# Optimization experiments

Hardware: AMD Instinct MI355X
Metric: run time of the kernel (lower is better)

The kernel has to match this reference:

```python
import jax, jax.numpy as jnp
import numpy as np
import math

L, B, S, D, H, DI, V = 4, 2, 1024, 768, 12, 3072, 512
DK = D // H

def gelu_tanh(x):
    c = math.sqrt(2.0 / math.pi)
    return 0.5 * x * (1.0 + jnp.tanh(c * (x + 0.044715 * x ** 3)))

def layer_norm(x, g, b, eps=1e-5):
    mu = jnp.mean(x, axis=-1, keepdims=True)
    var = jnp.var(x, axis=-1, keepdims=True)
    return (x - mu) * jax.lax.rsqrt(var + eps) * g + b

def setup_inputs() -> dict:
    key = jax.random.key(0)
    ks = jax.random.split(key, 12)
    w = 0.02  # init scale
    return {
        "x": jax.random.randint(ks[0], (B, S), 0, V),
        "embed": jax.random.normal(ks[1], (V, D), jnp.float32) * w,
        "pos_emb": jax.random.normal(ks[2], (S, D), jnp.float32) * w,
        "ln1_g": jnp.ones((L, D), jnp.float32),
        "ln1_b": jnp.zeros((L, D), jnp.float32),
        "wq": jax.random.normal(ks[3], (L, D, D), jnp.float32) * w,
        "bq": jnp.zeros((L, D), jnp.float32),
        "wk": jax.random.normal(ks[4], (L, D, D), jnp.float32) * w,
        "bk": jnp.zeros((L, D), jnp.float32),
        "wv": jax.random.normal(ks[5], (L, D, D), jnp.float32) * w,
        "bv": jnp.zeros((L, D), jnp.float32),
        "wo": jax.random.normal(ks[6], (L, D, D), jnp.float32) * w,
        "bo": jnp.zeros((L, D), jnp.float32),
        "ln2_g": jnp.ones((L, D), jnp.float32),
        "ln2_b": jnp.zeros((L, D), jnp.float32),
        "w_in": jax.random.normal(ks[7], (L, D, DI), jnp.float32) * w,
        "b_in": jnp.zeros((L, DI), jnp.float32),
        "w_out": jax.random.normal(ks[8], (L, DI, D), jnp.float32) * w,
        "b_out": jnp.zeros((L, D), jnp.float32),
        "lnf_g": jnp.ones((D,), jnp.float32),
        "lnf_b": jnp.zeros((D,), jnp.float32),
        "out_w": jax.random.normal(ks[9], (D, V), jnp.float32) * w,
    }

def reference(x, embed, pos_emb, ln1_g, ln1_b, wq, bq, wk, bk, wv, bv, wo, bo,
              ln2_g, ln2_b, w_in, b_in, w_out, b_out, lnf_g, lnf_b, out_w):
    s = x.shape[1]
    h = embed[x] + pos_emb[None, :s]                       # [B,S,D]
    causal = jnp.tril(jnp.ones((s, s), bool))              # True = keep
    scale = 1.0 / math.sqrt(DK)
    for l in range(L):
        a = layer_norm(h, ln1_g[l], ln1_b[l])
        q = (a @ wq[l] + bq[l]).reshape(-1, s, H, DK)
        k = (a @ wk[l] + bk[l]).reshape(-1, s, H, DK)
        v = (a @ wv[l] + bv[l]).reshape(-1, s, H, DK)
        scores = jnp.einsum('bqhd,bkhd->bhqk', q, k) * scale
        scores = jnp.where(causal, scores, -jnp.inf)
        attn = jax.nn.softmax(scores, axis=-1)
        o = jnp.einsum('bhqk,bkhd->bqhd', attn, v).reshape(-1, s, D)
        h = h + o @ wo[l] + bo[l]
        f = layer_norm(h, ln2_g[l], ln2_b[l])
        h = h + gelu_tanh(f @ w_in[l] + b_in[l]) @ w_out[l] + b_out[l]
    h = layer_norm(h, lnf_g, lnf_b)
    return h @ out_w                                       # [B,S,V] logits
```

## Files before the change

kernel.cpp:

```cpp
#include <hip/hip_runtime.h>
#include <hip/hip_bf16.h>


#define TKN    2048
#define DMODEL 768
#define SEQ    1024
#define NH     12
#define DHEAD  64
#define DFF    3072
#define NL     4
#define NVOCAB 512
#define NQKV   2304

typedef unsigned short u16;
typedef __attribute__((ext_vector_type(4))) float f32x4;
typedef __attribute__((ext_vector_type(8))) short short8;
typedef __attribute__((ext_vector_type(4))) unsigned short us4;
typedef __attribute__((ext_vector_type(8))) unsigned short us8;

__device__ __forceinline__ u16 f2bf(float f) {
  unsigned u = __builtin_bit_cast(unsigned, f);
  u += 0x7fffu + ((u >> 16) & 1u);
  return (u16)(u >> 16);
}

__device__ __forceinline__ float bf2f(u16 u) {
  unsigned v = ((unsigned)u) << 16;
  return __builtin_bit_cast(float, v);
}

__device__ __forceinline__ short8 mk8(us4 lo, us4 hi) {
  short8 r;
  r[0] = (short)lo[0]; r[1] = (short)lo[1]; r[2] = (short)lo[2]; r[3] = (short)lo[3];
  r[4] = (short)hi[0]; r[5] = (short)hi[1]; r[6] = (short)hi[2]; r[7] = (short)hi[3];
  return r;
}

__device__ __forceinline__ void gload16(const u16* g, u16* l) {
  __builtin_amdgcn_global_load_lds(
      (const __attribute__((address_space(1))) unsigned int*)g,
      (__attribute__((address_space(3))) unsigned int*)l, 16, 0, 0);
}

__global__ __launch_bounds__(256) void k_ln(const float* __restrict__ h,
                                            const float* __restrict__ gam,
                                            const float* __restrict__ bet,
                                            u16* __restrict__ out) {
  const int w = threadIdx.x >> 6, lane = threadIdx.x & 63;
  const int row = blockIdx.x * 4 + w;
  const float* hr = h + (size_t)row * DMODEL;
  float4 v0 = *(const float4*)(hr + lane * 4);
  float4 v1 = *(const float4*)(hr + 256 + lane * 4);
  float4 v2 = *(const float4*)(hr + 512 + lane * 4);
  float s = v0.x + v0.y + v0.z + v0.w + v1.x + v1.y + v1.z + v1.w
          + v2.x + v2.y + v2.z + v2.w;
#pragma unroll
  for (int off = 32; off > 0; off >>= 1) s += __shfl_xor(s, off);
  float mu = s * (1.0f / DMODEL);
  float d[12] = {v0.x - mu, v0.y - mu, v0.z - mu, v0.w - mu,
                 v1.x - mu, v1.y - mu, v1.z - mu, v1.w - mu,
                 v2.x - mu, v2.y - mu, v2.z - mu, v2.w - mu};
  float q = 0.0f;
#pragma unroll
  for (int i = 0; i < 12; ++i) q += d[i] * d[i];
#pragma unroll
  for (int off = 32; off > 0; off >>= 1) q += __shfl_xor(q, off);
  float rstd = rsqrtf(q * (1.0f / DMODEL) + 1e-5f);
  size_t o = (size_t)row * DMODEL;
#pragma unroll
  for (int j = 0; j < 3; ++j) {
    float4 gv = *(const float4*)(gam + j * 256 + lane * 4);
    float4 bv = *(const float4*)(bet + j * 256 + lane * 4);
    us4 ov;
    ov[0] = f2bf(d[j * 4 + 0] * rstd * gv.x + bv.x);
    ov[1] = f2bf(d[j * 4 + 1] * rstd * gv.y + bv.y);
    ov[2] = f2bf(d[j * 4 + 2] * rstd * gv.z + bv.z);
    ov[3] = f2bf(d[j * 4 + 3] * rstd * gv.w + bv.w);
    *(us4*)(out + o + j * 256 + lane * 4) = ov;
  }
}

__global__ __launch_bounds__(256) void k_pre(const float* __restrict__ wq,
                                             const float* __restrict__ wk,
                                             const float* __restrict__ wv,
                                             const float* __restrict__ wo,
                                             const float* __restrict__ win,
                                             const float* __restrict__ wout,
                                             const float* __restrict__ outw,
                                             const int* __restrict__ x,
                                             const float* __restrict__ emb,
                                             const float* __restrict__ pos,
                                             const float* __restrict__ bq,
                                             const float* __restrict__ bk,
                                             const float* __restrict__ bv,
                                             u16* __restrict__ wqkvT,
                                             u16* __restrict__ woT,
                                             u16* __restrict__ winT,
                                             u16* __restrict__ woutT,
                                             u16* __restrict__ outwT,
                                             float* __restrict__ h,
                                             float* __restrict__ bqkv) {
  const int l = blockIdx.y;
  const int t = blockIdx.x;
  const int tid = threadIdx.x, lane = tid & 63, w = tid >> 6;

  if (t >= 304) {
    if (l != 0) return;
    if (t == 560) {
      for (int i = tid; i < NL * NQKV; i += 256) {
        int ll = i / NQKV, j = i - ll * NQKV;
        float v = j < DMODEL ? bq[ll * DMODEL + j]
                : j < 2 * DMODEL ? bk[ll * DMODEL + j - DMODEL]
                : bv[ll * DMODEL + j - 2 * DMODEL];
        bqkv[i] = v;
      }
      return;
    }
    int e = t - 304;
#pragma unroll
    for (int tt = 0; tt < 2; ++tt) {
      int tok = e * 8 + w * 2 + tt;
      int s = tok & (SEQ - 1);
      int id = x[tok];
      const float* ep = emb + (size_t)id * DMODEL + lane * 4;
      const float* pp = pos + (size_t)s * DMODEL + lane * 4;
      float* hp = h + (size_t)tok * DMODEL + lane * 4;
#pragma unroll
      for (int j = 0; j < 3; ++j) {
        float4 a = *(const float4*)(ep + j * 256);
        float4 b = *(const float4*)(pp + j * 256);
        float4 o = {a.x + b.x, a.y + b.y, a.z + b.z, a.w + b.w};
        *(float4*)(hp + j * 256) = o;
      }
    }
    return;
  }

  const size_t wDD = (size_t)DMODEL * DMODEL, wDF = (size_t)DMODEL * DFF;
  const float* src; u16* dst;
  int ldS, ldD, scol0, n0, k0;
  if (t < 72) {
    int ntile = t >> 1, kc = t & 1;
    int gn0 = ntile * 64, sel = ntile / 12;
    src = (sel == 0 ? wq : sel == 1 ? wk : wv) + l * wDD; ldS = DMODEL;
    dst = wqkvT + l * (size_t)NQKV * DMODEL; ldD = DMODEL;
    scol0 = gn0 - sel * DMODEL; n0 = gn0; k0 = kc * 384;
  } else if (t < 96) {
    int t2 = t - 72, ntile = t2 >> 1, kc = t2 & 1;
    src = wo + l * wDD; ldS = DMODEL;
    dst = woT + l * wDD; ldD = DMODEL;
    scol0 = ntile * 64; n0 = ntile * 64; k0 = kc * 384;
  } else if (t < 192) {
    int t3 = t - 96, ntile = t3 >> 1, kc = t3 & 1;
    src = win + l * wDF; ldS = DFF;
    dst = winT + l * wDF; ldD = DMODEL;
    scol0 = ntile * 64; n0 = ntile * 64; k0 = kc * 384;
  } else if (t < 288) {
    int t4 = t - 192, ntile = t4 >> 3, kc = t4 & 7;
    src = wout + l * wDF; ldS = DMODEL;
    dst = woutT + l * wDF; ldD = DFF;
    scol0 = ntile * 64; n0 = ntile * 64; k0 = kc * 384;
  } else {
    if (l != 0) return;
    int t5 = t - 288, ntile = t5 >> 1, kc = t5 & 1;
    src = outw; ldS = NVOCAB;
    dst = outwT; ldD = DMODEL;
    scol0 = ntile * 64; n0 = ntile * 64; k0 = kc * 384;
  }
  const int R = lane >> 2, c = lane & 3;
#pragma unroll
  for (int ts = 0; ts < 3; ++ts) {
    const int kw = k0 + w * 96 + ts * 32 + c * 8;
    f32x4 v[8];
#pragma unroll
    for (int j = 0; j < 8; ++j)
      v[j] = *(const f32x4*)(src + (size_t)(kw + j) * ldS + scol0 + R * 4);
#pragma unroll
    for (int i = 0; i < 4; ++i) {
      u16 ob[8];
#pragma unroll
      for (int j = 0; j < 8; ++j) ob[j] = f2bf(v[j][i]);
      *(us8*)(dst + (size_t)(n0 + R * 4 + i) * ldD + kw) = *(us8*)ob;
    }
  }
}

template <int EP>
__global__ __launch_bounds__(256) void k_mm(const u16* __restrict__ A,
                                            const u16* __restrict__ BT,
                                            const float* __restrict__ bias,
                                            void* __restrict__ outp,
                                            int N, int K) {
  constexpr int BM = 64, BN = 64, MI = 2, NJ = 2;
  __shared__ __align__(16) u16 As[3][BM * 64];
  __shared__ __align__(16) u16 Bs[3][BN * 64];
  const int nbx = gridDim.x;
  int lin = blockIdx.y * nbx + blockIdx.x;
  const int chunk = (nbx * gridDim.y) >> 3;
  lin = (lin & 7) * chunk + (lin >> 3);
  const int bn = (lin % nbx) * BN, bm = (lin / nbx) * BM;

  const int tid = threadIdx.x, lane = tid & 63, wid = tid >> 6;
  const int g = lane >> 4, fl = lane & 15;
  const int wm = wid >> 1, wn = wid & 1;

  const int srow = wid * 8 + (lane >> 3);
  const int scol = ((lane & 7) ^ (lane >> 3)) << 3;
  const u16* ag = A + (size_t)(bm + srow) * K + scol;
  const u16* bg = BT + (size_t)(bn + srow) * K + scol;

  f32x4 acc[MI][NJ] = {};
  const int sw = (fl & 7) << 4;

  auto stage = [&](int buf, int kk) {
#pragma unroll
    for (int is = 0; is < MI; ++is)
      gload16(ag + kk + (size_t)is * 32 * K, &As[buf][wid * 512 + is * 2048]);
#pragma unroll
    for (int is = 0; is < NJ; ++is)
      gload16(bg + kk + (size_t)is * 32 * K, &Bs[buf][wid * 512 + is * 2048]);
  };

  const int ks = K / gridDim.z;
  const int kb0 = blockIdx.z * ks;
  const int nk = ks >> 6;
  stage(0, kb0);
  stage(1, kb0 + 64);
  asm volatile("s_waitcnt vmcnt(4)" ::: "memory");
  __builtin_amdgcn_s_barrier();

  int cur = 0, sbuf = 2;
  for (int kt = 0; kt < nk; ++kt) {
    if (kt + 2 < nk) {
      stage(sbuf, kb0 + ((kt + 2) << 6));
      sbuf = (sbuf == 2) ? 0 : sbuf + 1;
    }
#pragma unroll
    for (int k0 = 0; k0 < 64; k0 += 32) {
      const int bo = (k0 + 4 * g) * 2;
      short8 af[MI], bf[NJ];
#pragma unroll
      for (int i = 0; i < MI; ++i) {
        const char* base = (const char*)&As[cur][(wm * 32 + i * 16 + fl) * 64];
        af[i] = mk8(*(const us4*)(base + (bo ^ sw)),
                    *(const us4*)(base + ((bo + 32) ^ sw)));
      }
#pragma unroll
      for (int j = 0; j < NJ; ++j) {
        const char* base = (const char*)&Bs[cur][(wn * 32 + j * 16 + fl) * 64];
        bf[j] = mk8(*(const us4*)(base + (bo ^ sw)),
                    *(const us4*)(base + ((bo + 32) ^ sw)));
      }
#pragma unroll
      for (int i = 0; i < MI; ++i)
#pragma unroll
        for (int j = 0; j < NJ; ++j)
          acc[i][j] = __builtin_amdgcn_mfma_f32_16x16x32_bf16(af[i], bf[j], acc[i][j], 0, 0, 0);
    }
    cur = (cur == 2) ? 0 : cur + 1;
    if (kt + 1 < nk) {
      if (kt + 2 < nk)
        asm volatile("s_waitcnt vmcnt(4) lgkmcnt(0)" ::: "memory");
      else
        asm volatile("s_waitcnt vmcnt(0) lgkmcnt(0)" ::: "memory");
      __builtin_amdgcn_s_barrier();
    }
  }

  const int row0 = bm + wm * 32 + 4 * g;
  const int col0 = bn + wn * 32 + fl;
#pragma unroll
  for (int j = 0; j < NJ; ++j) {
    int col = col0 + j * 16;
    float bv = (EP == 3) ? 0.0f : bias[col];
    if (EP == 1 && blockIdx.z != 0) bv = 0.0f;
#pragma unroll
    for (int i = 0; i < MI; ++i) {
#pragma unroll
      for (int r = 0; r < 4; ++r) {
        int row = row0 + i * 16 + r;
        float val = acc[i][j][r] + bv;
        size_t idx = (size_t)row * N + col;
        if (EP == 0) {
          ((u16*)outp)[idx] = f2bf(val);
        } else if (EP == 1) {
          atomicAdd(&((float*)outp)[idx], val);
        } else if (EP == 2) {
          float t = 1.5957691216057308f * (val + 0.044715f * val * val * val);
          ((u16*)outp)[idx] = f2bf(val / (1.0f + __expf(-t)));
        } else if (EP == 3) {
          ((float*)outp)[idx] = val;
        } else {
          int sel = col / DMODEL;
          int cc = col - sel * DMODEL;
          int hh2 = cc >> 6, dk = cc & 63;
          int bb = row >> 10, ss = row & (SEQ - 1);
          if (sel == 0) val *= 0.125f;
          ((u16*)outp)[(size_t)sel * (TKN * DMODEL) +
                       (((size_t)(bb * NH + hh2) * SEQ + ss) << 6) + dk] = f2bf(val);
        }
      }
    }
  }
}

__global__ __launch_bounds__(256) void k_attn(const u16* __restrict__ qh,
                                              u16* __restrict__ pO,
                                              float* __restrict__ pML,
                                              u16* __restrict__ O) {
  __shared__ u16 Vt[DHEAD * 68];
  int bid = blockIdx.x;
  int lin = (bid & 7) * 120 + (bid >> 3);
  const int bh = lin / 40;
  const int idx = lin - bh * 40;
  int qb, sp;
  if (idx < 4)       { qb = idx;                     sp = 0; }
  else if (idx < 12) { qb = 4 + ((idx - 4) >> 1);    sp = (idx - 4) & 1; }
  else if (idx < 24) { int t = idx - 12; qb = 8 + t / 3;  sp = t - (t / 3) * 3; }
  else               { int t = idx - 24; qb = 12 + (t >> 2); sp = t & 3; }
  const int nsp = 1 + (qb >> 2), nt = qb + 1;
  const int t_lo = sp * nt / nsp, t_hi = (sp + 1) * nt / nsp;

  const int b = bh / NH, hh = bh % NH;
  const u16* kh = qh + TKN * DMODEL;
  const u16* vh = qh + 2 * (TKN * DMODEL);
  const size_t headbase = ((size_t)bh * SEQ) << 6;

  const int tid = threadIdx.x, lane = tid & 63, w = tid >> 6;
  const int g = lane >> 4, fl = lane & 15;
  const int qrow = qb * 64 + w * 16 + fl;

  short8 qf[2];
  {
    const u16* qp = qh + headbase + ((size_t)qrow << 6);
#pragma unroll
    for (int hf = 0; hf < 2; ++hf) {
      us4 lo = *(const us4*)(qp + hf * 32 + 4 * g);
      us4 hi = *(const us4*)(qp + hf * 32 + 16 + 4 * g);
      qf[hf] = mk8(lo, hi);
    }
  }

  float m = -1e30f, lsum = 0.0f;
  f32x4 oacc[4] = {};
  const int vr = tid >> 2, vd = (tid & 3) << 4;
  const u16* vbase = vh + headbase + ((size_t)vr << 6) + vd;
  const u16* kbase = kh + headbase;

  {
    const u16* vp = vbase + ((size_t)t_lo << 12);
    us4 vv[4];
#pragma unroll
    for (int qi = 0; qi < 4; ++qi) vv[qi] = *(const us4*)(vp + qi * 4);
#pragma unroll
    for (int qi = 0; qi < 4; ++qi)
#pragma unroll
      for (int i = 0; i < 4; ++i) Vt[(vd + qi * 4 + i) * 68 + vr] = vv[qi][i];
  }
  __syncthreads();

  for (int t64 = t_lo; t64 < t_hi; ++t64) {
    const u16* kb64 = kbase + ((size_t)t64 << 12);
    us4 kv[4][4];
#pragma unroll
    for (int q4 = 0; q4 < 4; ++q4) {
      const u16* kp = kb64 + ((q4 * 16 + fl) << 6);
#pragma unroll
      for (int j = 0; j < 4; ++j) kv[q4][j] = *(const us4*)(kp + j * 16 + 4 * g);
    }
    const bool pf = (t64 + 1 < t_hi);
    us4 vvn[4];
    if (pf) {
      const u16* vp = vbase + ((size_t)(t64 + 1) << 12);
#pragma unroll
      for (int qi = 0; qi < 4; ++qi) vvn[qi] = *(const us4*)(vp + qi * 4);
    }

    f32x4 sfr[4];
    __builtin_amdgcn_s_setprio(1);
#pragma unroll
    for (int sub = 0; sub < 4; ++sub) {
      short8 kf0 = mk8(kv[sub][0], kv[sub][1]);
      short8 kf1 = mk8(kv[sub][2], kv[sub][3]);
      f32x4 s = {};
      s = __builtin_amdgcn_mfma_f32_16x16x32_bf16(kf0, qf[0], s, 0, 0, 0);
      s = __builtin_amdgcn_mfma_f32_16x16x32_bf16(kf1, qf[1], s, 0, 0, 0);
      sfr[sub] = s;
    }
    __builtin_amdgcn_s_setprio(0);

    float sc[16];
    if (t64 == qb) {
#pragma unroll
      for (int sub = 0; sub < 4; ++sub)
#pragma unroll
        for (int r = 0; r < 4; ++r) {
          int key = t64 * 64 + sub * 16 + 4 * g + r;
          sc[sub * 4 + r] = (key <= qrow) ? sfr[sub][r] : -1e30f;
        }
    } else {
#pragma unroll
      for (int sub = 0; sub < 4; ++sub)
#pragma unroll
        for (int r = 0; r < 4; ++r) sc[sub * 4 + r] = sfr[sub][r];
    }
    float pmax = sc[0];
#pragma unroll
    for (int e = 1; e < 16; ++e) pmax = fmaxf(pmax, sc[e]);
    pmax = fmaxf(pmax, __shfl_xor(pmax, 16));
    pmax = fmaxf(pmax, __shfl_xor(pmax, 32));

    float p[16];
    if (__all(pmax <= m + 8.0f)) {
      float ps = 0.0f;
#pragma unroll
      for (int e = 0; e < 16; ++e) { p[e] = __expf(sc[e] - m); ps += p[e]; }
      ps += __shfl_xor(ps, 16);
      ps += __shfl_xor(ps, 32);
      lsum += ps;
    } else {
      float mnew = fmaxf(m, pmax);
      float corr = __expf(m - mnew);
      float ps = 0.0f;
#pragma unroll
      for (int e = 0; e < 16; ++e) { p[e] = __expf(sc[e] - mnew); ps += p[e]; }
      ps += __shfl_xor(ps, 16);
      ps += __shfl_xor(ps, 32);
      lsum = lsum * corr + ps;
      m = mnew;
      float cr[4];
#pragma unroll
      for (int r = 0; r < 4; ++r) cr[r] = __shfl(corr, 4 * g + r);
#pragma unroll
      for (int nb = 0; nb < 4; ++nb)
#pragma unroll
        for (int r = 0; r < 4; ++r) oacc[nb][r] *= cr[r];
    }

    short8 pf0, pf1;
#pragma unroll
    for (int e = 0; e < 8; ++e) { pf0[e] = (short)f2bf(p[e]); pf1[e] = (short)f2bf(p[8 + e]); }

    __builtin_amdgcn_s_setprio(1);
#pragma unroll
    for (int nb = 0; nb < 4; ++nb) {
      const u16* vtp = &Vt[(nb * 16 + fl) * 68 + 4 * g];
      short8 vf0 = mk8(*(const us4*)vtp, *(const us4*)(vtp + 16));
      short8 vf1 = mk8(*(const us4*)(vtp + 32), *(const us4*)(vtp + 48));
      oacc[nb] = __builtin_amdgcn_mfma_f32_16x16x32_bf16(pf0, vf0, oacc[nb], 0, 0, 0);
      oacc[nb] = __builtin_amdgcn_mfma_f32_16x16x32_bf16(pf1, vf1, oacc[nb], 0, 0, 0);
    }
    __builtin_amdgcn_s_setprio(0);

    if (pf) {
      __syncthreads();
#pragma unroll
      for (int qi = 0; qi < 4; ++qi)
#pragma unroll
        for (int i = 0; i < 4; ++i) Vt[(vd + qi * 4 + i) * 68 + vr] = vvn[qi][i];
      __syncthreads();
    }
  }

  if (nsp == 1) {
    float lr[4];
#pragma unroll
    for (int r = 0; r < 4; ++r) lr[r] = __shfl(lsum, 4 * g + r);
    const int orow0 = b * SEQ + qb * 64 + w * 16 + 4 * g;
#pragma unroll
    for (int nb = 0; nb < 4; ++nb) {
      int col = hh * DHEAD + nb * 16 + fl;
#pragma unroll
      for (int r = 0; r < 4; ++r)
        O[(size_t)(orow0 + r) * DMODEL + col] = f2bf(oacc[nb][r] / lr[r]);
    }
  } else {
    const size_t part = ((size_t)bh * 16 + qb) * 4 + sp;
    u16* ob = pO + part * 4096;
    float* ml = pML + part * 128;
#pragma unroll
    for (int nb = 0; nb < 4; ++nb)
#pragma unroll
      for (int r = 0; r < 4; ++r)
        ob[(w * 16 + 4 * g + r) * 64 + nb * 16 + fl] = f2bf(oacc[nb][r]);
    if (g == 0) {
      ml[w * 16 + fl] = m;
      ml[64 + w * 16 + fl] = lsum;
    }
  }
}

__global__ __launch_bounds__(256) void k_ared(const u16* __restrict__ pO,
                                              const float* __restrict__ pML,
                                              u16* __restrict__ O) {
  __shared__ float wgt[4][64];
  __shared__ float iLs[64];
  const int qb = blockIdx.x + 4, bh = blockIdx.y;
  const int nsp = 1 + (qb >> 2);
  const int b = bh / NH, hh = bh % NH;
  const int tid = threadIdx.x;
  const size_t p0 = ((size_t)bh * 16 + qb) * 4;
  if (tid < 64) {
    float M = -1e30f;
    for (int s = 0; s < nsp; ++s) M = fmaxf(M, pML[(p0 + s) * 128 + tid]);
    float L = 0.0f;
    for (int s = 0; s < nsp; ++s) {
      float wv = __expf(pML[(p0 + s) * 128 + tid] - M);
      wgt[s][tid] = wv;
      L += pML[(p0 + s) * 128 + 64 + tid] * wv;
    }
    iLs[tid] = 1.0f / L;
  }
  __syncthreads();
  for (int i = tid; i < 4096; i += 256) {
    int row = i >> 6, d = i & 63;
    float acc = 0.0f;
    for (int s = 0; s < nsp; ++s)
      acc += bf2f(pO[(p0 + s) * 4096 + i]) * wgt[s][row];
    O[(size_t)(b * SEQ + qb * 64 + row) * DMODEL + hh * DHEAD + d] = f2bf(acc * iLs[row]);
  }
}

extern "C" void kernel_launch(void* const* d_in, const int* in_sizes, int n_in,
                              void* d_out, int out_size, void* d_ws, size_t ws_size,
                              hipStream_t stream) {
  const int*   x    = (const int*)d_in[0];
  const float* emb  = (const float*)d_in[1];
  const float* pos  = (const float*)d_in[2];
  const float* ln1g = (const float*)d_in[3];
  const float* ln1b = (const float*)d_in[4];
  const float* wq   = (const float*)d_in[5];
  const float* bq   = (const float*)d_in[6];
  const float* wk   = (const float*)d_in[7];
  const float* bk   = (const float*)d_in[8];
  const float* wv   = (const float*)d_in[9];
  const float* bv   = (const float*)d_in[10];
  const float* wo   = (const float*)d_in[11];
  const float* bo   = (const float*)d_in[12];
  const float* ln2g = (const float*)d_in[13];
  const float* ln2b = (const float*)d_in[14];
  const float* win  = (const float*)d_in[15];
  const float* bin  = (const float*)d_in[16];
  const float* wout = (const float*)d_in[17];
  const float* bout = (const float*)d_in[18];
  const float* lnfg = (const float*)d_in[19];
  const float* lnfb = (const float*)d_in[20];
  const float* outw = (const float*)d_in[21];

  char* w8 = (char*)d_ws;
  float* h    = (float*)(w8);
  u16* abuf   = (u16*)(w8 + 6291456);
  float* pML  = (float*)(w8 + 6291456);
  u16* qkvh   = (u16*)(w8 + 9437184);
  u16* ffbuf  = (u16*)(w8 + 9437184);
  u16* obuf   = (u16*)(w8 + 18874368);
  u16* outwT  = (u16*)(w8 + 22020096);
  float* bqkv = (float*)(w8 + 22806528);
  u16* pO     = (u16*)(w8 + 22843392);
  u16* wqkvT  = (u16*)(w8 + 48009216);
  u16* woT    = (u16*)(w8 + 62164992);
  u16* winT   = (u16*)(w8 + 66883584);
  u16* woutT  = (u16*)(w8 + 85757952);

  const size_t wDD = (size_t)DMODEL * DMODEL, wDF = (size_t)DMODEL * DFF;
  const size_t wQKV = (size_t)NQKV * DMODEL;

  k_pre<<<dim3(561, NL), 256, 0, stream>>>(
      wq, wk, wv, wo, win, wout, outw, x, emb, pos, bq, bk, bv,
      wqkvT, woT, winT, woutT, outwT, h, bqkv);

  for (int l = 0; l < NL; ++l) {
    k_ln<<<TKN / 4, 256, 0, stream>>>(h, ln1g + l * DMODEL, ln1b + l * DMODEL, abuf);
    k_mm<4><<<dim3(NQKV / 64, TKN / 64, 1), 256, 0, stream>>>(
        abuf, wqkvT + l * wQKV, bqkv + l * NQKV, qkvh, NQKV, DMODEL);
    k_attn<<<960, 256, 0, stream>>>(qkvh, pO, pML, obuf);
    k_ared<<<dim3(12, 2 * NH), 256, 0, stream>>>(pO, pML, obuf);
    k_mm<1><<<dim3(DMODEL / 64, TKN / 64, 2), 256, 0, stream>>>(
        obuf, woT + l * wDD, bo + l * DMODEL, h, DMODEL, DMODEL);
    k_ln<<<TKN / 4, 256, 0, stream>>>(h, ln2g + l * DMODEL, ln2b + l * DMODEL, abuf);
    k_mm<2><<<dim3(DFF / 64, TKN / 64, 1), 256, 0, stream>>>(
        abuf, winT + l * wDF, bin + l * DFF, ffbuf, DFF, DMODEL);
    k_mm<1><<<dim3(DMODEL / 64, TKN / 64, 4), 256, 0, stream>>>(
        ffbuf, woutT + l * wDF, bout + l * DMODEL, h, DMODEL, DFF);
  }

  k_ln<<<TKN / 4, 256, 0, stream>>>(h, lnfg, lnfb, abuf);
  k_mm<3><<<dim3(NVOCAB / 64, TKN / 64, 1), 256, 0, stream>>>(
      abuf, outwT, nullptr, d_out, NVOCAB, DMODEL);
}
```

Baseline: 753.1 us.

## Enlarge GEMM M-tile to 128 with double-buffered pipeline and batch pre-kernel loads

Templates the bf16 MFMA GEMM on BM/BN and launches the layer GEMMs with 128x64 tiles, so each wave computes 4x2 MFMA fragments. This raises reuse of each loaded B tile and halves the block count. The shared-memory pipeline drops from three buffers with a two-stage prefetch and hand-tuned vmcnt waits to two buffers with __syncthreads, which frees LDS but may expose more load latency. The weight transpose/convert pre-kernel now issues all three sets of loads before converting, to get more memory-level parallelism.

```diff
diff --git a/kernel.cpp b/kernel.cpp
--- a/kernel.cpp
+++ b/kernel.cpp
@@ -168,32 +168,37 @@
     scol0 = ntile * 64; n0 = ntile * 64; k0 = kc * 384;
   }
   const int R = lane >> 2, c = lane & 3;
+  f32x4 v[3][8];
 #pragma unroll
   for (int ts = 0; ts < 3; ++ts) {
     const int kw = k0 + w * 96 + ts * 32 + c * 8;
-    f32x4 v[8];
 #pragma unroll
     for (int j = 0; j < 8; ++j)
-      v[j] = *(const f32x4*)(src + (size_t)(kw + j) * ldS + scol0 + R * 4);
+      v[ts][j] = *(const f32x4*)(src + (size_t)(kw + j) * ldS + scol0 + R * 4);
+  }
+#pragma unroll
+  for (int ts = 0; ts < 3; ++ts) {
+    const int kw = k0 + w * 96 + ts * 32 + c * 8;
 #pragma unroll
     for (int i = 0; i < 4; ++i) {
       u16 ob[8];
 #pragma unroll
-      for (int j = 0; j < 8; ++j) ob[j] = f2bf(v[j][i]);
+      for (int j = 0; j < 8; ++j) ob[j] = f2bf(v[ts][j][i]);
       *(us8*)(dst + (size_t)(n0 + R * 4 + i) * ldD + kw) = *(us8*)ob;
     }
   }
 }
 
-template <int EP>
+template <int EP, int BM, int BN>
 __global__ __launch_bounds__(256) void k_mm(const u16* __restrict__ A,
                                             const u16* __restrict__ BT,
                                             const float* __restrict__ bias,
                                             void* __restrict__ outp,
                                             int N, int K) {
-  constexpr int BM = 64, BN = 64, MI = 2, NJ = 2;
-  __shared__ __align__(16) u16 As[3][BM * 64];
-  __shared__ __align__(16) u16 Bs[3][BN * 64];
+  constexpr int MI = BM / 32;
+  constexpr int NJ = BN / 32;
+  __shared__ __align__(16) u16 As[2][BM * 64];
+  __shared__ __align__(16) u16 Bs[2][BN * 64];
   const int nbx = gridDim.x;
   int lin = blockIdx.y * nbx + blockIdx.x;
   const int chunk = (nbx * gridDim.y) >> 3;
@@ -225,29 +230,23 @@
   const int kb0 = blockIdx.z * ks;
   const int nk = ks >> 6;
   stage(0, kb0);
-  stage(1, kb0 + 64);
-  asm volatile("s_waitcnt vmcnt(4)" ::: "memory");
-  __builtin_amdgcn_s_barrier();
-
-  int cur = 0, sbuf = 2;
+  __syncthreads();
+  int cur = 0;
   for (int kt = 0; kt < nk; ++kt) {
-    if (kt + 2 < nk) {
-      stage(sbuf, kb0 + ((kt + 2) << 6));
-      sbuf = (sbuf == 2) ? 0 : sbuf + 1;
-    }
+    if (kt + 1 < nk) stage(cur ^ 1, kb0 + ((kt + 1) << 6));
 #pragma unroll
     for (int k0 = 0; k0 < 64; k0 += 32) {
       const int bo = (k0 + 4 * g) * 2;
       short8 af[MI], bf[NJ];
 #pragma unroll
       for (int i = 0; i < MI; ++i) {
-        const char* base = (const char*)&As[cur][(wm * 32 + i * 16 + fl) * 64];
+        const char* base = (const char*)&As[cur][(wm * (BM / 2) + i * 16 + fl) * 64];
         af[i] = mk8(*(const us4*)(base + (bo ^ sw)),
                     *(const us4*)(base + ((bo + 32) ^ sw)));
       }
 #pragma unroll
       for (int j = 0; j < NJ; ++j) {
-        const char* base = (const char*)&Bs[cur][(wn * 32 + j * 16 + fl) * 64];
+        const char* base = (const char*)&Bs[cur][(wn * (BN / 2) + j * 16 + fl) * 64];
         bf[j] = mk8(*(const us4*)(base + (bo ^ sw)),
                     *(const us4*)(base + ((bo + 32) ^ sw)));
       }
@@ -257,18 +256,12 @@
         for (int j = 0; j < NJ; ++j)
           acc[i][j] = __builtin_amdgcn_mfma_f32_16x16x32_bf16(af[i], bf[j], acc[i][j], 0, 0, 0);
     }
-    cur = (cur == 2) ? 0 : cur + 1;
-    if (kt + 1 < nk) {
-      if (kt + 2 < nk)
-        asm volatile("s_waitcnt vmcnt(4) lgkmcnt(0)" ::: "memory");
-      else
-        asm volatile("s_waitcnt vmcnt(0) lgkmcnt(0)" ::: "memory");
-      __builtin_amdgcn_s_barrier();
-    }
-  }
-
-  const int row0 = bm + wm * 32 + 4 * g;
-  const int col0 = bn + wn * 32 + fl;
+    __syncthreads();
+    cur ^= 1;
+  }
+
+  const int row0 = bm + wm * (BM / 2) + 4 * g;
+  const int col0 = bn + wn * (BN / 2) + fl;
 #pragma unroll
   for (int j = 0; j < NJ; ++j) {
     int col = col0 + j * 16;
@@ -571,20 +564,20 @@
 
   for (int l = 0; l < NL; ++l) {
     k_ln<<<TKN / 4, 256, 0, stream>>>(h, ln1g + l * DMODEL, ln1b + l * DMODEL, abuf);
-    k_mm<4><<<dim3(NQKV / 64, TKN / 64, 1), 256, 0, stream>>>(
+    k_mm<4, 128, 64><<<dim3(NQKV / 64, TKN / 128, 1), 256, 0, stream>>>(
         abuf, wqkvT + l * wQKV, bqkv + l * NQKV, qkvh, NQKV, DMODEL);
     k_attn<<<960, 256, 0, stream>>>(qkvh, pO, pML, obuf);
     k_ared<<<dim3(12, 2 * NH), 256, 0, stream>>>(pO, pML, obuf);
-    k_mm<1><<<dim3(DMODEL / 64, TKN / 64, 2), 256, 0, stream>>>(
+    k_mm<1, 128, 64><<<dim3(DMODEL / 64, TKN / 128, 2), 256, 0, stream>>>(
         obuf, woT + l * wDD, bo + l * DMODEL, h, DMODEL, DMODEL);
     k_ln<<<TKN / 4, 256, 0, stream>>>(h, ln2g + l * DMODEL, ln2b + l * DMODEL, abuf);
-    k_mm<2><<<dim3(DFF / 64, TKN / 64, 1), 256, 0, stream>>>(
+    k_mm<2, 128, 64><<<dim3(DFF / 64, TKN / 128, 1), 256, 0, stream>>>(
         abuf, winT + l * wDF, bin + l * DFF, ffbuf, DFF, DMODEL);
-    k_mm<1><<<dim3(DMODEL / 64, TKN / 64, 4), 256, 0, stream>>>(
+    k_mm<1, 128, 64><<<dim3(DMODEL / 64, TKN / 128, 4), 256, 0, stream>>>(
         ffbuf, woutT + l * wDF, bout + l * DMODEL, h, DMODEL, DFF);
   }
 
   k_ln<<<TKN / 4, 256, 0, stream>>>(h, lnfg, lnfb, abuf);
-  k_mm<3><<<dim3(NVOCAB / 64, TKN / 64, 1), 256, 0, stream>>>(
+  k_mm<3, 64, 64><<<dim3(NVOCAB / 64, TKN / 64, 1), 256, 0, stream>>>(
       abuf, outwT, nullptr, d_out, NVOCAB, DMODEL);
 }
```

Result: faster. 682.3 us (-9.4%).
